# Kernel optimization log

Hardware: AMD Instinct MI355X
Metric: run time of the kernel (lower is better)

The kernel has to match this reference:

```python
import jax, jax.numpy as jnp
import numpy as np

EPS = 1e-5

def setup_inputs() -> dict:
    key = jax.random.key(0)
    k1, k2, k3, k4, k5 = jax.random.split(key, 5)
    B, D, S = 4096, 2048, 16384
    return {
        "x": jax.random.normal(k1, (B, D), dtype=jnp.float32),
        "W_enc": jax.random.normal(k2, (S, D), dtype=jnp.float32) * 0.02,  # encoder.weight [n_sae, n_input]
        "W_dec": jax.random.normal(k3, (D, S), dtype=jnp.float32) * 0.02,  # decoder.weight [n_input, n_sae]
        "pre_bias": jax.random.normal(k4, (D,), dtype=jnp.float32) * 0.01,
        "sae_bias": jax.random.normal(k5, (S,), dtype=jnp.float32) * 0.01,
        "k": 64,
    }

def reference(x, W_enc, W_dec, pre_bias, sae_bias, k):
    # --- pre_process: layer norm (torch.std is unbiased -> ddof=1) ---
    x_mean = jnp.mean(x, axis=-1, keepdims=True)
    std = jnp.std(x, axis=-1, ddof=1, keepdims=True)
    x_ln = (x - x_mean) / (std + EPS)
    # --- encode: latents_pre = (x_ln - pre_bias) @ W_enc^T + sae_bias ---
    pre_activations = (x_ln - pre_bias) @ W_enc.T + sae_bias  # [B, n_sae]
    # --- TopK activation: keep top-k, ReLU them, zero the rest ---
    vals, idx = jax.lax.top_k(pre_activations, k)              # [B, k]
    vals = jax.nn.relu(vals)
    rows = jnp.arange(pre_activations.shape[0])[:, None]       # [B, 1]
    latents = jnp.zeros_like(pre_activations).at[rows, idx].set(vals)
    # --- decode + un-normalize ---
    recons = latents @ W_dec.T + pre_bias                      # [B, n_input]
    recons = recons * std + x_mean
    return pre_activations, latents, recons
```

## Files before the change

### kernel.cpp

```cpp
#include <hip/hip_runtime.h>
#include <cstdint>
#include <cstddef>

#define EPSV 1e-5f
#define CAP 224
#define PAD 16
#define DELTA 0.03f
#define AMBCAP 64

__device__ __forceinline__ unsigned short f2bf(float f) {
  unsigned u = __float_as_uint(f);
  unsigned r = (u + 0x7FFFu + ((u >> 16) & 1u)) >> 16;
  return (unsigned short)r;
}
__device__ __forceinline__ float bf2f(unsigned short h) {
  return __uint_as_float(((unsigned)h) << 16);
}

__global__ __launch_bounds__(256) void ln_kernel(const float* __restrict__ x,
    const float* __restrict__ pre_bias, float* __restrict__ a,
    unsigned short* __restrict__ A2,
    float* __restrict__ stats, int D) {
  const int b = blockIdx.x;
  const int tid = threadIdx.x;
  const float4* x4 = reinterpret_cast<const float4*>(x + (size_t)b * D);
  const float4* pb4 = reinterpret_cast<const float4*>(pre_bias);
  float4* a4 = reinterpret_cast<float4*>(a + (size_t)b * D);
  float4 v0 = x4[tid], v1 = x4[tid + 256];
  float s = v0.x + v0.y + v0.z + v0.w + v1.x + v1.y + v1.z + v1.w;
  float ss = v0.x*v0.x + v0.y*v0.y + v0.z*v0.z + v0.w*v0.w
           + v1.x*v1.x + v1.y*v1.y + v1.z*v1.z + v1.w*v1.w;
#pragma unroll
  for (int off = 1; off < 64; off <<= 1) { s += __shfl_xor(s, off); ss += __shfl_xor(ss, off); }
  __shared__ float wsum[4], wssq[4], bmean, bstd;
  int wave = tid >> 6;
  if ((tid & 63) == 0) { wsum[wave] = s; wssq[wave] = ss; }
  __syncthreads();
  if (tid == 0) {
    float S1 = wsum[0] + wsum[1] + wsum[2] + wsum[3];
    float S2 = wssq[0] + wssq[1] + wssq[2] + wssq[3];
    float mean = S1 / (float)D;
    float var = (S2 - (float)D * mean * mean) / (float)(D - 1);
    float sd = sqrtf(fmaxf(var, 0.f));
    bmean = mean; bstd = sd;
    stats[2*b] = mean; stats[2*b+1] = sd;
  }
  __syncthreads();
  float mean = bmean, rstd = 1.f / (bstd + EPSV);
  float4 p0 = pb4[tid], p1 = pb4[tid + 256];
  float4 o0, o1;
  o0.x = (v0.x - mean) * rstd - p0.x; o0.y = (v0.y - mean) * rstd - p0.y;
  o0.z = (v0.z - mean) * rstd - p0.z; o0.w = (v0.w - mean) * rstd - p0.w;
  o1.x = (v1.x - mean) * rstd - p1.x; o1.y = (v1.y - mean) * rstd - p1.y;
  o1.z = (v1.z - mean) * rstd - p1.z; o1.w = (v1.w - mean) * rstd - p1.w;
  a4[tid] = o0; a4[tid + 256] = o1;
  if (A2) {
    unsigned short* row = A2 + (size_t)b * 2048;
    ushort4 h0 = make_ushort4(f2bf(o0.x), f2bf(o0.y), f2bf(o0.z), f2bf(o0.w));
    ushort4 h1 = make_ushort4(f2bf(o1.x), f2bf(o1.y), f2bf(o1.z), f2bf(o1.w));
    *reinterpret_cast<ushort4*>(row + tid * 4) = h0;
    *reinterpret_cast<ushort4*>(row + 1024 + tid * 4) = h1;
  }
}

__global__ __launch_bounds__(256) void cvt_w_kernel(const float* __restrict__ W,
    unsigned short* __restrict__ W2, int D) {
  const int s = blockIdx.x, tid = threadIdx.x;
  const float4* w4 = reinterpret_cast<const float4*>(W + (size_t)s * D);
  unsigned short* row = W2 + (size_t)s * D;
  float4 v0 = w4[tid * 2], v1 = w4[tid * 2 + 1];
  uint4 p;
  p.x = (unsigned)f2bf(v0.x) | ((unsigned)f2bf(v0.y) << 16);
  p.y = (unsigned)f2bf(v0.z) | ((unsigned)f2bf(v0.w) << 16);
  p.z = (unsigned)f2bf(v1.x) | ((unsigned)f2bf(v1.y) << 16);
  p.w = (unsigned)f2bf(v1.z) | ((unsigned)f2bf(v1.w) << 16);
  *reinterpret_cast<uint4*>(row + tid * 8) = p;
}

typedef __attribute__((ext_vector_type(8))) short bf8;
typedef __attribute__((ext_vector_type(4))) float f32x4;

__device__ __forceinline__ void gload16(const void* g, void* l) {
  __builtin_amdgcn_global_load_lds(
      (const __attribute__((address_space(1))) unsigned int*)g,
      (__attribute__((address_space(3))) unsigned int*)l,
      16, 0, 0);
}

__global__ __launch_bounds__(512) void enc_gemm_bf16(
    const unsigned short* __restrict__ A2,
    const unsigned short* __restrict__ W2,
    const float* __restrict__ sae_bias,
    float* __restrict__ C, int M, int N) {
  __shared__ __align__(16) short As0[128 * 64];
  __shared__ __align__(16) short Bs0[128 * 64];
  __shared__ __align__(16) short As1[128 * 64];
  __shared__ __align__(16) short Bs1[128 * 64];
  const int tid = threadIdx.x;
  const int bn = blockIdx.x, bm = blockIdx.y;
  const int w = tid >> 6, l = tid & 63;

  const unsigned short* gA[2];
  const unsigned short* gB[2];
  int ldsSlot[2];
#pragma unroll
  for (int r = 0; r < 2; ++r) {
    int slot = r * 512 + tid;
    int row = slot >> 3, unit = slot & 7;
    int gcol = (unit ^ (row & 7)) * 8;
    gA[r] = A2 + (size_t)(bm * 128 + row) * 2048 + gcol;
    gB[r] = W2 + (size_t)(bn * 128 + row) * 2048 + gcol;
    ldsSlot[r] = slot * 8;
  }

  const int wm = (w >> 2) * 64, wn = (w & 3) * 32;
  const int r15 = l & 15, b7 = l & 7, u = l >> 4;
  const int colks0 = ((u + 0) ^ b7) * 8;
  const int colks1 = ((u + 4) ^ b7) * 8;
  const int baseA = (wm + r15) * 64;
  const int baseB = (wn + r15) * 64;

  f32x4 acc[4][2];
#pragma unroll
  for (int mi = 0; mi < 4; ++mi)
#pragma unroll
    for (int ni = 0; ni < 2; ++ni) acc[mi][ni] = (f32x4){0.f, 0.f, 0.f, 0.f};

#define STAGE(Adst, Bdst, koff)                                   \
  {                                                               \
    _Pragma("unroll")                                             \
    for (int r = 0; r < 2; ++r) {                                 \
      gload16(gA[r] + (koff), &(Adst)[ldsSlot[r]]);               \
      gload16(gB[r] + (koff), &(Bdst)[ldsSlot[r]]);               \
    }                                                             \
  }

#define COMPUTE(Asrc, Bsrc)                                       \
  {                                                               \
    bf8 af[8], bfv[4];                                            \
    _Pragma("unroll")                                             \
    for (int mi = 0; mi < 4; ++mi) {                              \
      af[mi]     = *reinterpret_cast<const bf8*>(&(Asrc)[baseA + mi * 1024 + colks0]); \
      af[4 + mi] = *reinterpret_cast<const bf8*>(&(Asrc)[baseA + mi * 1024 + colks1]); \
    }                                                             \
    _Pragma("unroll")                                             \
    for (int ni = 0; ni < 2; ++ni) {                              \
      bfv[ni]     = *reinterpret_cast<const bf8*>(&(Bsrc)[baseB + ni * 1024 + colks0]); \
      bfv[2 + ni] = *reinterpret_cast<const bf8*>(&(Bsrc)[baseB + ni * 1024 + colks1]); \
    }                                                             \
    __builtin_amdgcn_s_setprio(1);                                \
    _Pragma("unroll")                                             \
    for (int mi = 0; mi < 4; ++mi)                                \
      _Pragma("unroll")                                           \
      for (int ni = 0; ni < 2; ++ni)                              \
        acc[mi][ni] = __builtin_amdgcn_mfma_f32_16x16x32_bf16(    \
            af[mi], bfv[ni], acc[mi][ni], 0, 0, 0);               \
    _Pragma("unroll")                                             \
    for (int mi = 0; mi < 4; ++mi)                                \
      _Pragma("unroll")                                           \
      for (int ni = 0; ni < 2; ++ni)                              \
        acc[mi][ni] = __builtin_amdgcn_mfma_f32_16x16x32_bf16(    \
            af[4 + mi], bfv[2 + ni], acc[mi][ni], 0, 0, 0);       \
    __builtin_amdgcn_s_setprio(0);                                \
  }

#define SYNC_TILE()                                               \
  {                                                               \
    asm volatile("s_waitcnt vmcnt(0)" ::: "memory");              \
    __builtin_amdgcn_s_barrier();                                 \
    asm volatile("" ::: "memory");                                \
  }

  STAGE(As0, Bs0, 0);
  SYNC_TILE();

  for (int t = 0; t < 32; t += 2) {
    STAGE(As1, Bs1, (t + 1) * 64);
    COMPUTE(As0, Bs0);
    SYNC_TILE();
    if (t + 2 < 32) STAGE(As0, Bs0, (t + 2) * 64);
    COMPUTE(As1, Bs1);
    SYNC_TILE();
  }
#undef STAGE
#undef COMPUTE
#undef SYNC_TILE

  const int cm = (l >> 4) * 4, cn = l & 15;
  float sb[2];
#pragma unroll
  for (int ni = 0; ni < 2; ++ni)
    sb[ni] = sae_bias[bn * 128 + wn + ni * 16 + cn];
#pragma unroll
  for (int mi = 0; mi < 4; ++mi) {
#pragma unroll
    for (int r = 0; r < 4; ++r) {
      int row = bm * 128 + wm + mi * 16 + cm + r;
      float* Crow = C + (size_t)row * N + bn * 128 + wn;
#pragma unroll
      for (int ni = 0; ni < 2; ++ni)
        Crow[ni * 16 + cn] = acc[mi][ni][r] + sb[ni];
    }
  }
}

#define BM 128
#define BN 128
#define BK 32
#define LDP 136

__global__ __launch_bounds__(256) void enc_gemm_f32(
    const float* __restrict__ A, const float* __restrict__ Bw,
    const float* __restrict__ sae_bias, float* __restrict__ C,
    int M, int N, int K) {
  __shared__ __align__(16) float As[BK * LDP];
  __shared__ __align__(16) float Bs[BK * LDP];
  const int tid = threadIdx.x;
  const int bn = blockIdx.x, bm = blockIdx.y;
  const float* Ab = A + (size_t)bm * BM * K;
  const float* Bb = Bw + (size_t)bn * BN * K;
  float acc[8][8];
#pragma unroll
  for (int i = 0; i < 8; ++i)
#pragma unroll
    for (int j = 0; j < 8; ++j) acc[i][j] = 0.f;
  const int tn = tid & 15, tm = tid >> 4;
  const int lk = tid & 31;
  const int lm4 = (tid >> 5) * 4;
  for (int k0 = 0; k0 < K; k0 += BK) {
#pragma unroll
    for (int i = 0; i < 4; ++i) {
      int mb = i * 32 + lm4;
      float a0 = Ab[(size_t)(mb + 0) * K + k0 + lk];
      float a1 = Ab[(size_t)(mb + 1) * K + k0 + lk];
      float a2 = Ab[(size_t)(mb + 2) * K + k0 + lk];
      float a3 = Ab[(size_t)(mb + 3) * K + k0 + lk];
      *reinterpret_cast<float4*>(&As[lk * LDP + mb]) = make_float4(a0, a1, a2, a3);
      float b0 = Bb[(size_t)(mb + 0) * K + k0 + lk];
      float b1 = Bb[(size_t)(mb + 1) * K + k0 + lk];
      float b2 = Bb[(size_t)(mb + 2) * K + k0 + lk];
      float b3 = Bb[(size_t)(mb + 3) * K + k0 + lk];
      *reinterpret_cast<float4*>(&Bs[lk * LDP + mb]) = make_float4(b0, b1, b2, b3);
    }
    __syncthreads();
#pragma unroll 8
    for (int kk = 0; kk < BK; ++kk) {
      float4 a0 = *reinterpret_cast<const float4*>(&As[kk * LDP + tm * 4]);
      float4 a1 = *reinterpret_cast<const float4*>(&As[kk * LDP + tm * 4 + 64]);
      float4 b0 = *reinterpret_cast<const float4*>(&Bs[kk * LDP + tn * 4]);
      float4 b1 = *reinterpret_cast<const float4*>(&Bs[kk * LDP + tn * 4 + 64]);
      float av[8] = {a0.x, a0.y, a0.z, a0.w, a1.x, a1.y, a1.z, a1.w};
      float bv[8] = {b0.x, b0.y, b0.z, b0.w, b1.x, b1.y, b1.z, b1.w};
#pragma unroll
      for (int ii = 0; ii < 8; ++ii)
#pragma unroll
        for (int jj = 0; jj < 8; ++jj)
          acc[ii][jj] = fmaf(av[ii], bv[jj], acc[ii][jj]);
    }
    __syncthreads();
  }
  float4 sb0 = *reinterpret_cast<const float4*>(sae_bias + bn * BN + tn * 4);
  float4 sb1 = *reinterpret_cast<const float4*>(sae_bias + bn * BN + tn * 4 + 64);
#pragma unroll
  for (int ii = 0; ii < 8; ++ii) {
    int row = bm * BM + (ii < 4 ? tm * 4 + ii : 64 + tm * 4 + ii - 4);
    float* Crow = C + (size_t)row * N + bn * BN;
    float4 o0 = make_float4(acc[ii][0] + sb0.x, acc[ii][1] + sb0.y,
                            acc[ii][2] + sb0.z, acc[ii][3] + sb0.w);
    float4 o1 = make_float4(acc[ii][4] + sb1.x, acc[ii][5] + sb1.y,
                            acc[ii][6] + sb1.z, acc[ii][7] + sb1.w);
    *reinterpret_cast<float4*>(Crow + tn * 4) = o0;
    *reinterpret_cast<float4*>(Crow + tn * 4 + 64) = o1;
  }
}

__device__ __forceinline__ unsigned mapf(float f) {
  unsigned u = __float_as_uint(f);
  return (u & 0x80000000u) ? ~u : (u | 0x80000000u);
}

__global__ __launch_bounds__(256) void topk_select(
    const float* __restrict__ preact,
    const int* __restrict__ kp, int* __restrict__ cand, float* __restrict__ candv,
    int* __restrict__ candcnt, int S) {
  const int b = blockIdx.x, tid = threadIdx.x;
  const float4* row4 = reinterpret_cast<const float4*>(preact + (size_t)b * S);
  __shared__ int hist[4096];
  __shared__ int tsum[256];
  __shared__ unsigned sh_pref, sh_thr;
  __shared__ int sh_done, sh_cum, sh_cnt;
  int K = kp[0]; if (K > 192) K = 192;
  const int r = K + PAD;
  if (tid == 0) { sh_done = 0; sh_pref = 0; sh_cum = 0; }
  for (int level = 0; level < 3; ++level) {
    __syncthreads();
    if (sh_done) break;
    const int shift = (level == 0) ? 20 : (level == 1) ? 8 : 0;
    const int width = (level == 2) ? 8 : 12;
    const int nb = 1 << width;
    const unsigned mask = (unsigned)nb - 1;
    for (int i = tid; i < nb; i += 256) hist[i] = 0;
    __syncthreads();
    const unsigned pref = sh_pref;
    for (int i = tid; i < S / 4; i += 256) {
      float4 v = row4[i];
      unsigned uu[4] = {mapf(v.x), mapf(v.y), mapf(v.z), mapf(v.w)};
#pragma unroll
      for (int q = 0; q < 4; ++q) {
        bool ok = (level == 0) || ((uu[q] >> (shift + width)) == pref);
        if (ok) atomicAdd(&hist[(uu[q] >> shift) & mask], 1);
      }
    }
    __syncthreads();
    const int per = nb >> 8;
    int myts = 0;
#pragma unroll 4
    for (int j = 0; j < per; ++j) myts += hist[tid * per + j];
    tsum[tid] = myts;
    __syncthreads();
    for (int o = 1; o < 256; o <<= 1) {
      int v_ = (tid + o < 256) ? tsum[tid + o] : 0;
      __syncthreads();
      tsum[tid] += v_;
      __syncthreads();
    }
    const int rr = r - sh_cum;
    const int sufIncl = tsum[tid];
    const int sufExcl = sufIncl - myts;
    if (sufExcl < rr && rr <= sufIncl) {
      int running = sufExcl;
      for (int j = per - 1; j >= 0; --j) {
        int bb = tid * per + j;
        int c = hist[bb];
        if (running + c >= rr) {
          unsigned npref = (sh_pref << width) | (unsigned)bb;
          int candTotal = sh_cum + running + c;
          sh_pref = npref;
          sh_cum += running;
          if (candTotal <= CAP || level == 2) { sh_thr = npref << shift; sh_done = 1; }
          break;
        }
        running += c;
      }
    }
  }
  __syncthreads();
  const unsigned T = sh_thr;
  if (tid == 0) sh_cnt = 0;
  __syncthreads();
  for (int i = tid; i < S / 4; i += 256) {
    float4 v = row4[i];
    unsigned uu[4] = {mapf(v.x), mapf(v.y), mapf(v.z), mapf(v.w)};
    float vv[4] = {v.x, v.y, v.z, v.w};
#pragma unroll
    for (int q = 0; q < 4; ++q) {
      if (uu[q] >= T) {
        int p = atomicAdd(&sh_cnt, 1);
        if (p < CAP) { cand[(size_t)b * CAP + p] = i * 4 + q; candv[(size_t)b * CAP + p] = vv[q]; }
      }
    }
  }
  __syncthreads();
  if (tid == 0) candcnt[b] = (sh_cnt < CAP) ? sh_cnt : CAP;
}

__global__ __launch_bounds__(256) void topk_refine(
    const float* __restrict__ a, const float* __restrict__ W_enc,
    const float* __restrict__ sae_bias, const int* __restrict__ kp,
    const int* __restrict__ cand, const float* __restrict__ candv,
    const int* __restrict__ candcnt,
    float* __restrict__ latents, int* __restrict__ out_idx, float* __restrict__ out_val,
    int D, int S) {
  const int b = blockIdx.x, tid = threadIdx.x;
  __shared__ float sv[256];
  __shared__ int si[256];
  __shared__ double sv64[256];
  __shared__ double av[AMBCAP];
  __shared__ int agid[AMBCAP];
  __shared__ int sh_amb, sh_nin;
  int K = kp[0]; if (K > 192) K = 192;
  const int cnt = candcnt[b];
  const int wave = tid >> 6, lane = tid & 63;
  const float4* ar4 = reinterpret_cast<const float4*>(a + (size_t)b * D);
  const int nit = D / 256;

  if (tid < cnt) { sv[tid] = candv[(size_t)b * CAP + tid]; si[tid] = cand[(size_t)b * CAP + tid]; }
  else { sv[tid] = -3.0e38f; si[tid] = 0x7FFFFFFF; }
  __syncthreads();
  for (int ksz = 2; ksz <= 256; ksz <<= 1) {
    for (int j = ksz >> 1; j > 0; j >>= 1) {
      int ixj = tid ^ j;
      if (ixj > tid) {
        float v1 = sv[tid], v2 = sv[ixj];
        int i1 = si[tid], i2 = si[ixj];
        bool dirDesc = ((tid & ksz) == 0);
        bool firstBetter = (v1 > v2) || (v1 == v2 && i1 < i2);
        if (dirDesc ? (!firstBetter) : firstBetter) {
          sv[tid] = v2; sv[ixj] = v1; si[tid] = i2; si[ixj] = i1;
        }
      }
      __syncthreads();
    }
  }
  const float vK = sv[K - 1];
  if (tid == 0) { sh_amb = 0; sh_nin = 0; }
  __syncthreads();
  bool isC = tid < cnt;
  if (isC && (sv[tid] > vK + DELTA)) atomicAdd(&sh_nin, 1);
  if (isC && fabsf(sv[tid] - vK) <= DELTA) {
    int p = atomicAdd(&sh_amb, 1);
    if (p < AMBCAP) agid[p] = si[tid];
  }
  __syncthreads();
  const int nAmb = sh_amb, nIn = sh_nin;

  if (nAmb <= AMBCAP) {
    for (int c = wave; c < nAmb; c += 4) {
      int sidx = agid[c];
      const float4* wr4 = reinterpret_cast<const float4*>(W_enc + (size_t)sidx * D);
      double acc = 0.0;
      for (int m = 0; m < nit; ++m) {
        float4 a_ = ar4[m * 64 + lane];
        float4 w_ = wr4[m * 64 + lane];
        acc += (double)a_.x * w_.x + (double)a_.y * w_.y
             + (double)a_.z * w_.z + (double)a_.w * w_.w;
      }
#pragma unroll
      for (int off = 1; off < 64; off <<= 1) acc += __shfl_xor(acc, off);
      if (lane == 0) av[c] = acc + (double)sae_bias[sidx];
    }
    __syncthreads();
    if (tid < AMBCAP && tid >= nAmb) { av[tid] = -1.0e300; agid[tid] = 0x7FFFFFFF; }
    __syncthreads();
    for (int ksz = 2; ksz <= AMBCAP; ksz <<= 1) {
      for (int j = ksz >> 1; j > 0; j >>= 1) {
        int ixj = tid ^ j;
        if (tid < AMBCAP && ixj > tid) {
          double v1 = av[tid], v2 = av[ixj];
          int i1 = agid[tid], i2 = agid[ixj];
          bool dirDesc = ((tid & ksz) == 0);
          bool firstBetter = (v1 > v2) || (v1 == v2 && i1 < i2);
          if (dirDesc ? (!firstBetter) : firstBetter) {
            av[tid] = v2; av[ixj] = v1; agid[tid] = i2; agid[ixj] = i1;
          }
        }
        __syncthreads();
      }
    }
    if (tid < K) {
      int gidx; float val;
      if (tid < nIn) { gidx = si[tid]; val = sv[tid]; }
      else { int c = tid - nIn; gidx = agid[c]; val = (float)av[c]; }
      val = fmaxf(val, 0.f);
      latents[(size_t)b * S + gidx] = val;
      out_idx[(size_t)b * 256 + tid] = gidx;
      out_val[(size_t)b * 256 + tid] = val;
    }
  } else {
    for (int c = wave; c < cnt; c += 4) {
      int sidx = si[c];
      const float4* wr4 = reinterpret_cast<const float4*>(W_enc + (size_t)sidx * D);
      double acc = 0.0;
      for (int m = 0; m < nit; ++m) {
        float4 a_ = ar4[m * 64 + lane];
        float4 w_ = wr4[m * 64 + lane];
        acc += (double)a_.x * w_.x + (double)a_.y * w_.y
             + (double)a_.z * w_.z + (double)a_.w * w_.w;
      }
#pragma unroll
      for (int off = 1; off < 64; off <<= 1) acc += __shfl_xor(acc, off);
      if (lane == 0) sv64[c] = acc + (double)sae_bias[sidx];
    }
    __syncthreads();
    if (tid >= cnt) { sv64[tid] = -1.0e300; si[tid] = 0x7FFFFFFF; }
    __syncthreads();
    for (int ksz = 2; ksz <= 256; ksz <<= 1) {
      for (int j = ksz >> 1; j > 0; j >>= 1) {
        int ixj = tid ^ j;
        if (ixj > tid) {
          double v1 = sv64[tid], v2 = sv64[ixj];
          int i1 = si[tid], i2 = si[ixj];
          bool dirDesc = ((tid & ksz) == 0);
          bool firstBetter = (v1 > v2) || (v1 == v2 && i1 < i2);
          if (dirDesc ? (!firstBetter) : firstBetter) {
            sv64[tid] = v2; sv64[ixj] = v1; si[tid] = i2; si[ixj] = i1;
          }
        }
        __syncthreads();
      }
    }
    if (tid < K) {
      int idx = si[tid];
      float rv = fmaxf((float)sv64[tid], 0.f);
      latents[(size_t)b * S + idx] = rv;
      out_idx[(size_t)b * 256 + tid] = idx;
      out_val[(size_t)b * 256 + tid] = rv;
    }
  }
}

__global__ __launch_bounds__(256) void transpose_cvt(const float* __restrict__ src,
    unsigned short* __restrict__ dst, int D, int S) {
  __shared__ float t[32][33];
  int s0 = blockIdx.x * 32, d0 = blockIdx.y * 32;
  int tx = threadIdx.x & 31, ty = threadIdx.x >> 5;
#pragma unroll
  for (int i = 0; i < 32; i += 8)
    t[ty + i][tx] = src[(size_t)(d0 + ty + i) * S + s0 + tx];
  __syncthreads();
#pragma unroll
  for (int i = 0; i < 32; i += 8)
    dst[(size_t)(s0 + ty + i) * D + d0 + tx] = f2bf(t[tx][ty + i]);
}

__global__ __launch_bounds__(512) void decode_bf16(
    const unsigned short* __restrict__ WdTh, const float* __restrict__ pre_bias,
    const float* __restrict__ stats, const int* __restrict__ kp,
    const int* __restrict__ out_idx, const float* __restrict__ out_val,
    float* __restrict__ recons, int D) {
  const int b = blockIdx.x, tid = threadIdx.x;
  __shared__ int sidx[192];
  __shared__ float sval[192];
  int K = kp[0]; if (K > 192) K = 192;
  if (tid < K) { sidx[tid] = out_idx[(size_t)b * 256 + tid]; sval[tid] = out_val[(size_t)b * 256 + tid]; }
  __syncthreads();
  const int c0 = tid * 4;
  float4 p0 = *reinterpret_cast<const float4*>(pre_bias + c0);
  float acc0 = p0.x, acc1 = p0.y, acc2 = p0.z, acc3 = p0.w;
  for (int j = 0; j < K; ++j) {
    float v = sval[j];
    uint2 wv = *reinterpret_cast<const uint2*>(WdTh + (size_t)sidx[j] * D + c0);
    acc0 = fmaf(v, bf2f((unsigned short)(wv.x & 0xffff)), acc0);
    acc1 = fmaf(v, bf2f((unsigned short)(wv.x >> 16)),    acc1);
    acc2 = fmaf(v, bf2f((unsigned short)(wv.y & 0xffff)), acc2);
    acc3 = fmaf(v, bf2f((unsigned short)(wv.y >> 16)),    acc3);
  }
  float mean = stats[2 * b], sd = stats[2 * b + 1];
  float4 o = make_float4(acc0 * sd + mean, acc1 * sd + mean,
                         acc2 * sd + mean, acc3 * sd + mean);
  *reinterpret_cast<float4*>(recons + (size_t)b * D + c0) = o;
}

__global__ __launch_bounds__(256) void decode_fb(
    const float* __restrict__ Wd, const float* __restrict__ pre_bias,
    const float* __restrict__ stats, const int* __restrict__ kp,
    const int* __restrict__ out_idx, const float* __restrict__ out_val,
    float* __restrict__ recons, int D, int S) {
  const int b = blockIdx.x, tid = threadIdx.x;
  __shared__ int sidx[192];
  __shared__ float sval[192];
  int K = kp[0]; if (K > 192) K = 192;
  if (tid < K) { sidx[tid] = out_idx[(size_t)b * 256 + tid]; sval[tid] = out_val[(size_t)b * 256 + tid]; }
  __syncthreads();
  for (int d = tid; d < D; d += 256) {
    float acc = pre_bias[d];
    for (int j = 0; j < K; ++j)
      acc = fmaf(sval[j], Wd[(size_t)d * S + sidx[j]], acc);
    recons[(size_t)b * D + d] = acc * stats[2 * b + 1] + stats[2 * b];
  }
}

extern "C" void kernel_launch(void* const* d_in, const int* in_sizes, int n_in,
                              void* d_out, int out_size, void* d_ws, size_t ws_size,
                              hipStream_t stream) {
  const float* x        = (const float*)d_in[0];
  const float* W_enc    = (const float*)d_in[1];
  const float* W_dec    = (const float*)d_in[2];
  const float* pre_bias = (const float*)d_in[3];
  const float* sae_bias = (const float*)d_in[4];
  const int*   kp       = (const int*)d_in[5];
  const int D = in_sizes[3];
  const int S = in_sizes[4];
  const int B = in_sizes[0] / D;

  float* out_pre = (float*)d_out;
  float* out_lat = out_pre + (size_t)B * S;
  float* out_rec = out_lat + (size_t)B * S;

  char* ws = (char*)d_ws;
  size_t off = 0;
  float* a = (float*)(ws + off);        off += (size_t)B * D * 4;
  float* stats = (float*)(ws + off);    off += (size_t)B * 2 * 4;
  int* cand = (int*)(ws + off);         off += (size_t)B * CAP * 4;
  float* candv = (float*)(ws + off);    off += (size_t)B * CAP * 4;
  int* candcnt = (int*)(ws + off);      off += (size_t)B * 4;
  int* oidx = (int*)(ws + off);         off += (size_t)B * 256 * 4;
  float* oval = (float*)(ws + off);     off += (size_t)B * 256 * 4;
  off = (off + 255) & ~(size_t)255;
  unsigned short* A2 = (unsigned short*)(ws + off);
  size_t offW2 = off + (size_t)B * D * 2;
  unsigned short* W2 = (unsigned short*)(ws + offW2);
  size_t offWdT = offW2 + (size_t)S * D * 2;
  unsigned short* WdTh = (unsigned short*)(ws + offWdT);
  size_t offEnd = offWdT + (size_t)S * D * 2;
  bool useBf16 = (D == 2048) && (B % 128 == 0) && (S % 128 == 0) &&
                 (S % 32 == 0) && (D % 32 == 0) && (ws_size >= offEnd);

  hipMemsetAsync(out_lat, 0, (size_t)B * S * 4, stream);

  if (useBf16) {
    ln_kernel<<<B, 256, 0, stream>>>(x, pre_bias, a, A2, stats, D);
    cvt_w_kernel<<<S, 256, 0, stream>>>(W_enc, W2, D);
    enc_gemm_bf16<<<dim3(S / 128, B / 128), 512, 0, stream>>>(A2, W2, sae_bias, out_pre, B, S);
    transpose_cvt<<<dim3(S / 32, D / 32), 256, 0, stream>>>(W_dec, WdTh, D, S);
    topk_select<<<B, 256, 0, stream>>>(out_pre, kp, cand, candv, candcnt, S);
    topk_refine<<<B, 256, 0, stream>>>(a, W_enc, sae_bias, kp, cand, candv, candcnt,
                                       out_lat, oidx, oval, D, S);
    decode_bf16<<<B, 512, 0, stream>>>(WdTh, pre_bias, stats, kp, oidx, oval, out_rec, D);
  } else {
    ln_kernel<<<B, 256, 0, stream>>>(x, pre_bias, a, nullptr, stats, D);
    enc_gemm_f32<<<dim3(S / BN, B / BM), 256, 0, stream>>>(a, W_enc, sae_bias, out_pre, B, S, D);
    topk_select<<<B, 256, 0, stream>>>(out_pre, kp, cand, candv, candcnt, S);
    topk_refine<<<B, 256, 0, stream>>>(a, W_enc, sae_bias, kp, cand, candv, candcnt,
                                       out_lat, oidx, oval, D, S);
    decode_fb<<<B, 256, 0, stream>>>(W_dec, pre_bias, stats, kp, oidx, oval, out_rec, D, S);
  }
}
```

Measured before the change: 846.7 us.

## Prepack activations into MFMA fragment layout and load A directly from global

```diff
diff --git a/kernel.cpp b/kernel.cpp
--- a/kernel.cpp
+++ b/kernel.cpp
@@ -63,6 +63,18 @@
   }
 }
 
+__global__ __launch_bounds__(256) void repack_a(const unsigned short* __restrict__ A2,
+    unsigned short* __restrict__ A2F) {
+  const int mt = blockIdx.x;
+  const int tid = threadIdx.x;
+  for (int idx = tid; idx < 64 * 64; idx += 256) {
+    int kc = idx >> 6, l = idx & 63;
+    const unsigned short* src = A2 + (size_t)(mt * 16 + (l & 15)) * 2048 + kc * 32 + (l >> 4) * 8;
+    unsigned short* dst = A2F + ((size_t)mt * 64 + kc) * 512 + (size_t)l * 8;
+    *reinterpret_cast<uint4*>(dst) = *reinterpret_cast<const uint4*>(src);
+  }
+}
+
 __global__ __launch_bounds__(256) void cvt_w_kernel(const float* __restrict__ W,
     unsigned short* __restrict__ W2, int D) {
   const int s = blockIdx.x, tid = threadIdx.x;
@@ -88,19 +100,16 @@
 }
 
 __global__ __launch_bounds__(512) void enc_gemm_bf16(
-    const unsigned short* __restrict__ A2,
+    const unsigned short* __restrict__ A2F,
     const unsigned short* __restrict__ W2,
     const float* __restrict__ sae_bias,
     float* __restrict__ C, int M, int N) {
-  __shared__ __align__(16) short As0[128 * 64];
   __shared__ __align__(16) short Bs0[128 * 64];
-  __shared__ __align__(16) short As1[128 * 64];
   __shared__ __align__(16) short Bs1[128 * 64];
   const int tid = threadIdx.x;
   const int bn = blockIdx.x, bm = blockIdx.y;
   const int w = tid >> 6, l = tid & 63;
 
-  const unsigned short* gA[2];
   const unsigned short* gB[2];
   int ldsSlot[2];
 #pragma unroll
@@ -108,7 +117,6 @@
     int slot = r * 512 + tid;
     int row = slot >> 3, unit = slot & 7;
     int gcol = (unit ^ (row & 7)) * 8;
-    gA[r] = A2 + (size_t)(bm * 128 + row) * 2048 + gcol;
     gB[r] = W2 + (size_t)(bn * 128 + row) * 2048 + gcol;
     ldsSlot[r] = slot * 8;
   }
@@ -117,31 +125,30 @@
   const int r15 = l & 15, b7 = l & 7, u = l >> 4;
   const int colks0 = ((u + 0) ^ b7) * 8;
   const int colks1 = ((u + 4) ^ b7) * 8;
-  const int baseA = (wm + r15) * 64;
   const int baseB = (wn + r15) * 64;
 
+  const unsigned short* gAF = A2F + ((size_t)(bm * 8 + (wm >> 4)) * 64) * 512 + (size_t)l * 8;
+
   f32x4 acc[4][2];
 #pragma unroll
   for (int mi = 0; mi < 4; ++mi)
 #pragma unroll
     for (int ni = 0; ni < 2; ++ni) acc[mi][ni] = (f32x4){0.f, 0.f, 0.f, 0.f};
 
-#define STAGE(Adst, Bdst, koff)                                   \
+#define STAGEB(Bdst, koff)                                        \
   {                                                               \
     _Pragma("unroll")                                             \
-    for (int r = 0; r < 2; ++r) {                                 \
-      gload16(gA[r] + (koff), &(Adst)[ldsSlot[r]]);               \
+    for (int r = 0; r < 2; ++r)                                   \
       gload16(gB[r] + (koff), &(Bdst)[ldsSlot[r]]);               \
-    }                                                             \
-  }
-
-#define COMPUTE(Asrc, Bsrc)                                       \
+  }
+
+#define COMPUTE(Bsrc, t)                                          \
   {                                                               \
     bf8 af[8], bfv[4];                                            \
     _Pragma("unroll")                                             \
     for (int mi = 0; mi < 4; ++mi) {                              \
-      af[mi]     = *reinterpret_cast<const bf8*>(&(Asrc)[baseA + mi * 1024 + colks0]); \
-      af[4 + mi] = *reinterpret_cast<const bf8*>(&(Asrc)[baseA + mi * 1024 + colks1]); \
+      af[mi]     = *reinterpret_cast<const bf8*>(gAF + ((size_t)mi * 64 + 2 * (t)) * 512);     \
+      af[4 + mi] = *reinterpret_cast<const bf8*>(gAF + ((size_t)mi * 64 + 2 * (t) + 1) * 512); \
     }                                                             \
     _Pragma("unroll")                                             \
     for (int ni = 0; ni < 2; ++ni) {                              \
@@ -171,18 +178,18 @@
     asm volatile("" ::: "memory");                                \
   }
 
-  STAGE(As0, Bs0, 0);
+  STAGEB(Bs0, 0);
   SYNC_TILE();
 
   for (int t = 0; t < 32; t += 2) {
-    STAGE(As1, Bs1, (t + 1) * 64);
-    COMPUTE(As0, Bs0);
+    STAGEB(Bs1, (t + 1) * 64);
+    COMPUTE(Bs0, t);
     SYNC_TILE();
-    if (t + 2 < 32) STAGE(As0, Bs0, (t + 2) * 64);
-    COMPUTE(As1, Bs1);
+    if (t + 2 < 32) STAGEB(Bs0, (t + 2) * 64);
+    COMPUTE(Bs1, t + 1);
     SYNC_TILE();
   }
-#undef STAGE
+#undef STAGEB
 #undef COMPUTE
 #undef SYNC_TILE
 
@@ -588,20 +595,23 @@
   float* oval = (float*)(ws + off);     off += (size_t)B * 256 * 4;
   off = (off + 255) & ~(size_t)255;
   unsigned short* A2 = (unsigned short*)(ws + off);
-  size_t offW2 = off + (size_t)B * D * 2;
+  size_t offA2F = off + (size_t)B * D * 2;
+  unsigned short* A2F = (unsigned short*)(ws + offA2F);
+  size_t offW2 = offA2F + (size_t)B * D * 2;
   unsigned short* W2 = (unsigned short*)(ws + offW2);
   size_t offWdT = offW2 + (size_t)S * D * 2;
   unsigned short* WdTh = (unsigned short*)(ws + offWdT);
   size_t offEnd = offWdT + (size_t)S * D * 2;
-  bool useBf16 = (D == 2048) && (B % 128 == 0) && (S % 128 == 0) &&
-                 (S % 32 == 0) && (D % 32 == 0) && (ws_size >= offEnd);
+  bool useBf16 = (D == 2048) && (B % 128 == 0) && (B % 16 == 0) &&
+                 (S % 128 == 0) && (S % 32 == 0) && (ws_size >= offEnd);
 
   hipMemsetAsync(out_lat, 0, (size_t)B * S * 4, stream);
 
   if (useBf16) {
     ln_kernel<<<B, 256, 0, stream>>>(x, pre_bias, a, A2, stats, D);
+    repack_a<<<B / 16, 256, 0, stream>>>(A2, A2F);
     cvt_w_kernel<<<S, 256, 0, stream>>>(W_enc, W2, D);
-    enc_gemm_bf16<<<dim3(S / 128, B / 128), 512, 0, stream>>>(A2, W2, sae_bias, out_pre, B, S);
+    enc_gemm_bf16<<<dim3(S / 128, B / 128), 512, 0, stream>>>(A2F, W2, sae_bias, out_pre, B, S);
     transpose_cvt<<<dim3(S / 32, D / 32), 256, 0, stream>>>(W_dec, WdTh, D, S);
     topk_select<<<B, 256, 0, stream>>>(out_pre, kp, cand, candv, candcnt, S);
     topk_refine<<<B, 256, 0, stream>>>(a, W_enc, sae_bias, kp, cand, candv, candcnt,
```

Result: slower. 923.5 us (+9.1%).
